# Kernel tuning notes

Hardware: AMD Instinct MI355X
Metric: run time of the kernel (lower is better)

The kernel has to match this reference:

```python
import jax, jax.numpy as jnp
import numpy as np

NUM_HEADS = 32      # query heads
NUM_KV_HEADS = 8    # GQA kv heads
HEAD_DIM = 128
BS = 16             # decode batch (one new token per sequence)
KV_LEN = 2048       # pages (page_size=1 -> tokens) per sequence
NUM_SLOTS = BS * KV_LEN
SCALE = HEAD_DIM ** -0.5


def setup_inputs() -> dict:
    key = jax.random.key(0)
    ks = jax.random.split(key, 6)
    q = jax.random.normal(ks[0], (BS, NUM_HEADS * HEAD_DIM), dtype=jnp.float32)
    k = jax.random.normal(ks[1], (BS, NUM_KV_HEADS * HEAD_DIM), dtype=jnp.float32)
    v = jax.random.normal(ks[2], (BS, NUM_KV_HEADS * HEAD_DIM), dtype=jnp.float32)
    k_cache = jax.random.normal(ks[3], (NUM_SLOTS, NUM_KV_HEADS * HEAD_DIM), dtype=jnp.float32)
    v_cache = jax.random.normal(ks[4], (NUM_SLOTS, NUM_KV_HEADS * HEAD_DIM), dtype=jnp.float32)
    # paged layout: each sequence owns KV_LEN non-contiguous slots (page_size=1)
    perm = jax.random.permutation(ks[5], NUM_SLOTS).astype(jnp.int32)
    page_indices = perm.reshape(BS, KV_LEN)            # [BS, KV_LEN] slot ids
    slot_mapping = page_indices[:, -1]                 # new token written to last page
    return {"q": q, "k": k, "v": v, "k_cache": k_cache, "v_cache": v_cache,
            "slot_mapping": slot_mapping, "page_indices": page_indices}


def reference(q, k, v, k_cache, v_cache, slot_mapping, page_indices):
    # store_kvcache: scatter new K/V rows into flat [num_slots, Hkv*d] caches
    k_cache = k_cache.at[slot_mapping].set(k)
    v_cache = v_cache.at[slot_mapping].set(v)
    # paged gather (page_size=1): [BS, KV_LEN, Hkv, d]
    keys = k_cache[page_indices].reshape(BS, KV_LEN, NUM_KV_HEADS, HEAD_DIM)
    vals = v_cache[page_indices].reshape(BS, KV_LEN, NUM_KV_HEADS, HEAD_DIM)
    # GQA: query head h uses kv head h // group
    group = NUM_HEADS // NUM_KV_HEADS
    qh = q.reshape(BS, NUM_KV_HEADS, group, HEAD_DIM)
    scores = jnp.einsum('bhgd,blhd->bhgl', qh, keys) * SCALE   # [BS,Hkv,g,L]
    p = jax.nn.softmax(scores, axis=-1)
    o = jnp.einsum('bhgl,blhd->bhgd', p, vals)                 # [BS,Hkv,g,d]
    return o.reshape(BS, NUM_HEADS * HEAD_DIM)
```

## Files before the change

### kernel.cpp

```cpp
#include <hip/hip_runtime.h>
#include <math.h>

constexpr int NUM_HEADS    = 32;
constexpr int NUM_KV_HEADS = 8;
constexpr int HEAD_DIM     = 128;
constexpr int BS           = 16;
constexpr int KV_LEN       = 2048;
constexpr int GROUP        = NUM_HEADS / NUM_KV_HEADS;
constexpr int NCHUNK       = 8;
constexpr int CHUNK        = KV_LEN / NCHUNK;

__global__ __launch_bounds__(256, 4) void attn_partial_kernel(
    const float* __restrict__ q,
    const float* __restrict__ knew,
    const float* __restrict__ vnew,
    const float* __restrict__ k_cache,
    const float* __restrict__ v_cache,
    const int*   __restrict__ page_indices,
    float* __restrict__ ws_o,
    float* __restrict__ ws_m,
    float* __restrict__ ws_s)
{
    const int bid   = blockIdx.x;
    const int chunk = bid % NCHUNK;
    const int h     = (bid / NCHUNK) % NUM_KV_HEADS;
    const int b     = bid / (NCHUNK * NUM_KV_HEADS);

    const int tid  = threadIdx.x;
    const int wid  = tid >> 6;
    const int lane = tid & 63;
    const int g    = lane >> 4;
    const int sub  = lane & 15;

    const float qscale = 0.08838834764831845f * 1.4426950408889634f;

    float qv[GROUP][8];
#pragma unroll
    for (int hg = 0; hg < GROUP; ++hg) {
        const float* qp = q + ((size_t)b * NUM_HEADS + h * GROUP + hg) * HEAD_DIM;
        const float4 a = *(const float4*)(qp + sub * 4);
        const float4 c = *(const float4*)(qp + 64 + sub * 4);
        qv[hg][0] = a.x * qscale; qv[hg][1] = a.y * qscale;
        qv[hg][2] = a.z * qscale; qv[hg][3] = a.w * qscale;
        qv[hg][4] = c.x * qscale; qv[hg][5] = c.y * qscale;
        qv[hg][6] = c.z * qscale; qv[hg][7] = c.w * qscale;
    }

    float m[GROUP], ssum[GROUP], o[GROUP][8];
#pragma unroll
    for (int hg = 0; hg < GROUP; ++hg) {
        m[hg] = -INFINITY; ssum[hg] = 0.f;
#pragma unroll
        for (int j = 0; j < 8; ++j) o[hg][j] = 0.f;
    }

    const int lbase = chunk * CHUNK;
    const float* knew_row = knew + ((size_t)b * NUM_KV_HEADS + h) * HEAD_DIM;
    const float* vnew_row = vnew + ((size_t)b * NUM_KV_HEADS + h) * HEAD_DIM;

    for (int it = 0; it < CHUNK / 16; ++it) {
        const int l   = lbase + it * 16 + wid * 4 + g;
        const int idx = page_indices[b * KV_LEN + l];

        const float* kr;
        const float* vr;
        if (l == KV_LEN - 1) {
            kr = knew_row; vr = vnew_row;
        } else {
            kr = k_cache + ((size_t)idx * NUM_KV_HEADS + h) * HEAD_DIM;
            vr = v_cache + ((size_t)idx * NUM_KV_HEADS + h) * HEAD_DIM;
        }
        const float4 k0 = *(const float4*)(kr + sub * 4);
        const float4 k1 = *(const float4*)(kr + 64 + sub * 4);
        const float4 v0 = *(const float4*)(vr + sub * 4);
        const float4 v1 = *(const float4*)(vr + 64 + sub * 4);

        float sc[GROUP];
#pragma unroll
        for (int hg = 0; hg < GROUP; ++hg) {
            sc[hg] = qv[hg][0] * k0.x + qv[hg][1] * k0.y + qv[hg][2] * k0.z + qv[hg][3] * k0.w
                   + qv[hg][4] * k1.x + qv[hg][5] * k1.y + qv[hg][6] * k1.z + qv[hg][7] * k1.w;
        }
#pragma unroll
        for (int off = 1; off < 16; off <<= 1) {
#pragma unroll
            for (int hg = 0; hg < GROUP; ++hg)
                sc[hg] += __shfl_xor(sc[hg], off, 64);
        }
#pragma unroll
        for (int hg = 0; hg < GROUP; ++hg) {
            const float mn = fmaxf(m[hg], sc[hg]);
            const float cf = exp2f(m[hg] - mn);
            const float pr = exp2f(sc[hg] - mn);
            ssum[hg] = ssum[hg] * cf + pr;
            m[hg] = mn;
            o[hg][0] = o[hg][0] * cf + pr * v0.x;
            o[hg][1] = o[hg][1] * cf + pr * v0.y;
            o[hg][2] = o[hg][2] * cf + pr * v0.z;
            o[hg][3] = o[hg][3] * cf + pr * v0.w;
            o[hg][4] = o[hg][4] * cf + pr * v1.x;
            o[hg][5] = o[hg][5] * cf + pr * v1.y;
            o[hg][6] = o[hg][6] * cf + pr * v1.z;
            o[hg][7] = o[hg][7] * cf + pr * v1.w;
        }
    }

#pragma unroll
    for (int off = 16; off <= 32; off <<= 1) {
#pragma unroll
        for (int hg = 0; hg < GROUP; ++hg) {
            const float mo = __shfl_xor(m[hg], off, 64);
            const float so = __shfl_xor(ssum[hg], off, 64);
            float oo[8];
#pragma unroll
            for (int j = 0; j < 8; ++j) oo[j] = __shfl_xor(o[hg][j], off, 64);
            const float mn = fmaxf(m[hg], mo);
            const float c1 = exp2f(m[hg] - mn);
            const float c2 = exp2f(mo - mn);
            ssum[hg] = ssum[hg] * c1 + so * c2;
#pragma unroll
            for (int j = 0; j < 8; ++j) o[hg][j] = o[hg][j] * c1 + oo[j] * c2;
            m[hg] = mn;
        }
    }

    __shared__ float red_o[4][GROUP][HEAD_DIM];
    __shared__ float red_m[4][GROUP];
    __shared__ float red_s[4][GROUP];
    if (lane < 16) {
#pragma unroll
        for (int hg = 0; hg < GROUP; ++hg) {
            *(float4*)&red_o[wid][hg][sub * 4]      = make_float4(o[hg][0], o[hg][1], o[hg][2], o[hg][3]);
            *(float4*)&red_o[wid][hg][64 + sub * 4] = make_float4(o[hg][4], o[hg][5], o[hg][6], o[hg][7]);
        }
        if (sub == 0) {
#pragma unroll
            for (int hg = 0; hg < GROUP; ++hg) { red_m[wid][hg] = m[hg]; red_s[wid][hg] = ssum[hg]; }
        }
    }
    __syncthreads();

    if (wid == 0) {
        const int hg = g;
        const float mn = fmaxf(fmaxf(red_m[0][hg], red_m[1][hg]),
                               fmaxf(red_m[2][hg], red_m[3][hg]));
        float stot = 0.f;
        float acc[8] = {0.f,0.f,0.f,0.f,0.f,0.f,0.f,0.f};
#pragma unroll
        for (int w = 0; w < 4; ++w) {
            const float c = exp2f(red_m[w][hg] - mn);
            stot += red_s[w][hg] * c;
#pragma unroll
            for (int j = 0; j < 4; ++j) acc[j]     += red_o[w][hg][sub * 4 + j] * c;
#pragma unroll
            for (int j = 0; j < 4; ++j) acc[4 + j] += red_o[w][hg][64 + sub * 4 + j] * c;
        }
        const size_t pbase = (((size_t)chunk * BS + b) * NUM_KV_HEADS + h) * GROUP + hg;
        float* op = ws_o + pbase * HEAD_DIM;
        *(float4*)(op + sub * 4)      = make_float4(acc[0], acc[1], acc[2], acc[3]);
        *(float4*)(op + 64 + sub * 4) = make_float4(acc[4], acc[5], acc[6], acc[7]);
        if (sub == 0) { ws_m[pbase] = mn; ws_s[pbase] = stot; }
    }
}

__global__ __launch_bounds__(128) void attn_combine_kernel(
    const float* __restrict__ ws_o,
    const float* __restrict__ ws_m,
    const float* __restrict__ ws_s,
    float* __restrict__ out)
{
    const int bid = blockIdx.x;
    const int hg  = bid % GROUP;
    const int h   = (bid / GROUP) % NUM_KV_HEADS;
    const int b   = bid / (GROUP * NUM_KV_HEADS);
    const int d   = threadIdx.x;

    float mv[NCHUNK];
    float mx = -INFINITY;
#pragma unroll
    for (int c = 0; c < NCHUNK; ++c) {
        mv[c] = ws_m[(((size_t)c * BS + b) * NUM_KV_HEADS + h) * GROUP + hg];
        mx = fmaxf(mx, mv[c]);
    }
    float stot = 0.f, acc = 0.f;
#pragma unroll
    for (int c = 0; c < NCHUNK; ++c) {
        const size_t pbase = (((size_t)c * BS + b) * NUM_KV_HEADS + h) * GROUP + hg;
        const float cf = exp2f(mv[c] - mx);
        stot += ws_s[pbase] * cf;
        acc  += ws_o[pbase * HEAD_DIM + d] * cf;
    }
    out[((size_t)b * NUM_HEADS + h * GROUP + hg) * HEAD_DIM + d] = acc / stot;
}

extern "C" void kernel_launch(void* const* d_in, const int* in_sizes, int n_in,
                              void* d_out, int out_size, void* d_ws, size_t ws_size,
                              hipStream_t stream)
{
    const float* q       = (const float*)d_in[0];
    const float* k       = (const float*)d_in[1];
    const float* v       = (const float*)d_in[2];
    const float* k_cache = (const float*)d_in[3];
    const float* v_cache = (const float*)d_in[4];
    const int* page_indices = (const int*)d_in[6];
    float* out = (float*)d_out;

    float* ws_o = (float*)d_ws;
    float* ws_m = ws_o + (size_t)NCHUNK * BS * NUM_KV_HEADS * GROUP * HEAD_DIM;
    float* ws_s = ws_m + (size_t)NCHUNK * BS * NUM_KV_HEADS * GROUP;

    attn_partial_kernel<<<BS * NUM_KV_HEADS * NCHUNK, 256, 0, stream>>>(
        q, k, v, k_cache, v_cache, page_indices, ws_o, ws_m, ws_s);
    attn_combine_kernel<<<BS * NUM_KV_HEADS * GROUP, 128, 0, stream>>>(
        ws_o, ws_m, ws_s, out);
}
```

Measured before the change: 50.71 us.

## Double the KV split, preload page indices, and software-prefetch next K/V rows

Doubles the number of KV chunks to 16, which halves the per-block loop length and doubles the grid to 2048 blocks for more memory parallelism. All page indices a thread needs are loaded into registers up front, and the loop is fully unrolled with the next iteration's K/V float4 loads issued before the current iteration's compute. The goal is to hide gather latency on the random paged accesses. In exchange it raises register pressure, which could limit occupancy under launch_bounds(256,4), and doubles the partial workspace that the combine kernel reads.

```diff
diff --git a/kernel.cpp b/kernel.cpp
--- a/kernel.cpp
+++ b/kernel.cpp
@@ -7,8 +7,9 @@
 constexpr int BS           = 16;
 constexpr int KV_LEN       = 2048;
 constexpr int GROUP        = NUM_HEADS / NUM_KV_HEADS;
-constexpr int NCHUNK       = 8;
+constexpr int NCHUNK       = 16;
 constexpr int CHUNK        = KV_LEN / NCHUNK;
+constexpr int NIT          = CHUNK / 16;
 
 __global__ __launch_bounds__(256, 4) void attn_partial_kernel(
     const float* __restrict__ q,
@@ -31,6 +32,14 @@
     const int lane = tid & 63;
     const int g    = lane >> 4;
     const int sub  = lane & 15;
+    const int lg   = wid * 4 + g;
+
+    const int lbase = chunk * CHUNK;
+
+    int idxr[NIT];
+#pragma unroll
+    for (int it = 0; it < NIT; ++it)
+        idxr[it] = page_indices[b * KV_LEN + lbase + it * 16 + lg];
 
     const float qscale = 0.08838834764831845f * 1.4426950408889634f;
 
@@ -46,34 +55,47 @@
         qv[hg][6] = c.z * qscale; qv[hg][7] = c.w * qscale;
     }
 
-    float m[GROUP], ssum[GROUP], o[GROUP][8];
-#pragma unroll
-    for (int hg = 0; hg < GROUP; ++hg) {
-        m[hg] = -INFINITY; ssum[hg] = 0.f;
-#pragma unroll
-        for (int j = 0; j < 8; ++j) o[hg][j] = 0.f;
-    }
-
-    const int lbase = chunk * CHUNK;
     const float* knew_row = knew + ((size_t)b * NUM_KV_HEADS + h) * HEAD_DIM;
     const float* vnew_row = vnew + ((size_t)b * NUM_KV_HEADS + h) * HEAD_DIM;
 
-    for (int it = 0; it < CHUNK / 16; ++it) {
-        const int l   = lbase + it * 16 + wid * 4 + g;
-        const int idx = page_indices[b * KV_LEN + l];
-
-        const float* kr;
-        const float* vr;
+    auto make_ptrs = [&](int it, const float*& kr, const float*& vr) {
+        const int l   = lbase + it * 16 + lg;
+        const int idx = idxr[it];
         if (l == KV_LEN - 1) {
             kr = knew_row; vr = vnew_row;
         } else {
             kr = k_cache + ((size_t)idx * NUM_KV_HEADS + h) * HEAD_DIM;
             vr = v_cache + ((size_t)idx * NUM_KV_HEADS + h) * HEAD_DIM;
         }
-        const float4 k0 = *(const float4*)(kr + sub * 4);
-        const float4 k1 = *(const float4*)(kr + 64 + sub * 4);
-        const float4 v0 = *(const float4*)(vr + sub * 4);
-        const float4 v1 = *(const float4*)(vr + 64 + sub * 4);
+    };
+
+    float m[GROUP], ssum[GROUP], o[GROUP][8];
+#pragma unroll
+    for (int hg = 0; hg < GROUP; ++hg) {
+        m[hg] = -INFINITY; ssum[hg] = 0.f;
+#pragma unroll
+        for (int j = 0; j < 8; ++j) o[hg][j] = 0.f;
+    }
+
+    float4 k0, k1, v0, v1;
+    {
+        const float *kr, *vr; make_ptrs(0, kr, vr);
+        k0 = *(const float4*)(kr + sub * 4);
+        k1 = *(const float4*)(kr + 64 + sub * 4);
+        v0 = *(const float4*)(vr + sub * 4);
+        v1 = *(const float4*)(vr + 64 + sub * 4);
+    }
+
+#pragma unroll
+    for (int it = 0; it < NIT; ++it) {
+        float4 nk0, nk1, nv0, nv1;
+        if (it + 1 < NIT) {
+            const float *kr, *vr; make_ptrs(it + 1, kr, vr);
+            nk0 = *(const float4*)(kr + sub * 4);
+            nk1 = *(const float4*)(kr + 64 + sub * 4);
+            nv0 = *(const float4*)(vr + sub * 4);
+            nv1 = *(const float4*)(vr + 64 + sub * 4);
+        }
 
         float sc[GROUP];
 #pragma unroll
@@ -103,6 +125,8 @@
             o[hg][6] = o[hg][6] * cf + pr * v1.z;
             o[hg][7] = o[hg][7] * cf + pr * v1.w;
         }
+
+        if (it + 1 < NIT) { k0 = nk0; k1 = nk1; v0 = nv0; v1 = nv1; }
     }
 
 #pragma unroll
```

Measured after the change: 122.0 us. +140.6%, slower.

## Stage full KV rows into LDS via async global_load_lds with double buffering

Applied to the files above, without the earlier changes.

Each block now covers one sequence and chunk across all 8 KV heads, with one wave per head. Whole K/V cache rows (all heads) are copied into LDS using global_load_lds DMA, double-buffered, with page indices prefetched one step ahead. The aim is to read each page row contiguously, overlap memory traffic with compute, and cut redundant index loads. In exchange there is a block-wide barrier every 4 positions and an extra cross-wave reduction in the combine step, since NCHUNK grows to 32 and per-wave partials are written straight out.

```diff
diff --git a/kernel.cpp b/kernel.cpp
--- a/kernel.cpp
+++ b/kernel.cpp
@@ -7,10 +7,20 @@
 constexpr int BS           = 16;
 constexpr int KV_LEN       = 2048;
 constexpr int GROUP        = NUM_HEADS / NUM_KV_HEADS;
-constexpr int NCHUNK       = 8;
+constexpr int NCHUNK       = 32;
 constexpr int CHUNK        = KV_LEN / NCHUNK;
-
-__global__ __launch_bounds__(256, 4) void attn_partial_kernel(
+constexpr int TPOS         = 4;
+constexpr int NT           = CHUNK / TPOS;
+constexpr int ROWF         = NUM_KV_HEADS * HEAD_DIM;
+constexpr int POSSTRIDE    = 2 * ROWF + 8;
+
+__device__ __forceinline__ void dma16(const float* g, float* l) {
+    __builtin_amdgcn_global_load_lds(
+        (const __attribute__((address_space(1))) void*)g,
+        (__attribute__((address_space(3))) void*)l, 16, 0, 0);
+}
+
+__global__ __launch_bounds__(512, 2) void attn_partial_kernel(
     const float* __restrict__ q,
     const float* __restrict__ knew,
     const float* __restrict__ vnew,
@@ -23,14 +33,20 @@
 {
     const int bid   = blockIdx.x;
     const int chunk = bid % NCHUNK;
-    const int h     = (bid / NCHUNK) % NUM_KV_HEADS;
-    const int b     = bid / (NCHUNK * NUM_KV_HEADS);
+    const int b     = bid / NCHUNK;
 
     const int tid  = threadIdx.x;
     const int wid  = tid >> 6;
     const int lane = tid & 63;
     const int g    = lane >> 4;
     const int sub  = lane & 15;
+    const int h    = wid;
+    const int arr  = wid >> 2;
+    const int quar = wid & 3;
+
+    const int lbase = chunk * CHUNK;
+
+    __shared__ float smem[2][TPOS][POSSTRIDE];
 
     const float qscale = 0.08838834764831845f * 1.4426950408889634f;
 
@@ -54,26 +70,48 @@
         for (int j = 0; j < 8; ++j) o[hg][j] = 0.f;
     }
 
-    const int lbase = chunk * CHUNK;
-    const float* knew_row = knew + ((size_t)b * NUM_KV_HEADS + h) * HEAD_DIM;
-    const float* vnew_row = vnew + ((size_t)b * NUM_KV_HEADS + h) * HEAD_DIM;
-
-    for (int it = 0; it < CHUNK / 16; ++it) {
-        const int l   = lbase + it * 16 + wid * 4 + g;
-        const int idx = page_indices[b * KV_LEN + l];
-
-        const float* kr;
-        const float* vr;
-        if (l == KV_LEN - 1) {
-            kr = knew_row; vr = vnew_row;
-        } else {
-            kr = k_cache + ((size_t)idx * NUM_KV_HEADS + h) * HEAD_DIM;
-            vr = v_cache + ((size_t)idx * NUM_KV_HEADS + h) * HEAD_DIM;
-        }
-        const float4 k0 = *(const float4*)(kr + sub * 4);
-        const float4 k1 = *(const float4*)(kr + 64 + sub * 4);
-        const float4 v0 = *(const float4*)(vr + sub * 4);
-        const float4 v1 = *(const float4*)(vr + 64 + sub * 4);
+    const float* kcnew = knew + (size_t)b * ROWF;
+    const float* vcnew = vnew + (size_t)b * ROWF;
+
+    auto stage = [&](int buf, int t, const int idx[TPOS]) {
+#pragma unroll
+        for (int j = 0; j < TPOS; ++j) {
+            const int l = lbase + t * TPOS + j;
+            const float* src;
+            if (l == KV_LEN - 1)
+                src = arr ? vcnew : kcnew;
+            else
+                src = (arr ? v_cache : k_cache) + (size_t)idx[j] * ROWF;
+            dma16(src + quar * 256 + lane * 4,
+                  &smem[buf][j][arr * ROWF + quar * 256]);
+        }
+    };
+
+    int nidx[TPOS];
+#pragma unroll
+    for (int j = 0; j < TPOS; ++j) nidx[j] = page_indices[b * KV_LEN + lbase + j];
+    stage(0, 0, nidx);
+#pragma unroll
+    for (int j = 0; j < TPOS; ++j) nidx[j] = page_indices[b * KV_LEN + lbase + TPOS + j];
+
+#pragma unroll 1
+    for (int t = 0; t < NT; ++t) {
+        __syncthreads();
+
+        if (t + 1 < NT) {
+            stage((t + 1) & 1, t + 1, nidx);
+            if (t + 2 < NT) {
+#pragma unroll
+                for (int j = 0; j < TPOS; ++j)
+                    nidx[j] = page_indices[b * KV_LEN + lbase + (t + 2) * TPOS + j];
+            }
+        }
+
+        const float* bp = &smem[t & 1][g][0];
+        const float4 k0 = *(const float4*)(bp + h * HEAD_DIM + sub * 4);
+        const float4 k1 = *(const float4*)(bp + h * HEAD_DIM + 64 + sub * 4);
+        const float4 v0 = *(const float4*)(bp + ROWF + h * HEAD_DIM + sub * 4);
+        const float4 v1 = *(const float4*)(bp + ROWF + h * HEAD_DIM + 64 + sub * 4);
 
         float sc[GROUP];
 #pragma unroll
@@ -124,42 +162,18 @@
         }
     }
 
-    __shared__ float red_o[4][GROUP][HEAD_DIM];
-    __shared__ float red_m[4][GROUP];
-    __shared__ float red_s[4][GROUP];
     if (lane < 16) {
-#pragma unroll
-        for (int hg = 0; hg < GROUP; ++hg) {
-            *(float4*)&red_o[wid][hg][sub * 4]      = make_float4(o[hg][0], o[hg][1], o[hg][2], o[hg][3]);
-            *(float4*)&red_o[wid][hg][64 + sub * 4] = make_float4(o[hg][4], o[hg][5], o[hg][6], o[hg][7]);
+        const size_t pb0 = (((size_t)chunk * BS + b) * NUM_KV_HEADS + h) * GROUP;
+#pragma unroll
+        for (int hg = 0; hg < GROUP; ++hg) {
+            float* op = ws_o + (pb0 + hg) * HEAD_DIM;
+            *(float4*)(op + sub * 4)      = make_float4(o[hg][0], o[hg][1], o[hg][2], o[hg][3]);
+            *(float4*)(op + 64 + sub * 4) = make_float4(o[hg][4], o[hg][5], o[hg][6], o[hg][7]);
         }
         if (sub == 0) {
 #pragma unroll
-            for (int hg = 0; hg < GROUP; ++hg) { red_m[wid][hg] = m[hg]; red_s[wid][hg] = ssum[hg]; }
-        }
-    }
-    __syncthreads();
-
-    if (wid == 0) {
-        const int hg = g;
-        const float mn = fmaxf(fmaxf(red_m[0][hg], red_m[1][hg]),
-                               fmaxf(red_m[2][hg], red_m[3][hg]));
-        float stot = 0.f;
-        float acc[8] = {0.f,0.f,0.f,0.f,0.f,0.f,0.f,0.f};
-#pragma unroll
-        for (int w = 0; w < 4; ++w) {
-            const float c = exp2f(red_m[w][hg] - mn);
-            stot += red_s[w][hg] * c;
-#pragma unroll
-            for (int j = 0; j < 4; ++j) acc[j]     += red_o[w][hg][sub * 4 + j] * c;
-#pragma unroll
-            for (int j = 0; j < 4; ++j) acc[4 + j] += red_o[w][hg][64 + sub * 4 + j] * c;
-        }
-        const size_t pbase = (((size_t)chunk * BS + b) * NUM_KV_HEADS + h) * GROUP + hg;
-        float* op = ws_o + pbase * HEAD_DIM;
-        *(float4*)(op + sub * 4)      = make_float4(acc[0], acc[1], acc[2], acc[3]);
-        *(float4*)(op + 64 + sub * 4) = make_float4(acc[4], acc[5], acc[6], acc[7]);
-        if (sub == 0) { ws_m[pbase] = mn; ws_s[pbase] = stot; }
+            for (int hg = 0; hg < GROUP; ++hg) { ws_m[pb0 + hg] = m[hg]; ws_s[pb0 + hg] = ssum[hg]; }
+        }
     }
 }
 
@@ -175,18 +189,17 @@
     const int b   = bid / (GROUP * NUM_KV_HEADS);
     const int d   = threadIdx.x;
 
-    float mv[NCHUNK];
     float mx = -INFINITY;
-#pragma unroll
+#pragma unroll 8
     for (int c = 0; c < NCHUNK; ++c) {
-        mv[c] = ws_m[(((size_t)c * BS + b) * NUM_KV_HEADS + h) * GROUP + hg];
-        mx = fmaxf(mx, mv[c]);
+        const float mv = ws_m[(((size_t)c * BS + b) * NUM_KV_HEADS + h) * GROUP + hg];
+        mx = fmaxf(mx, mv);
     }
     float stot = 0.f, acc = 0.f;
-#pragma unroll
+#pragma unroll 8
     for (int c = 0; c < NCHUNK; ++c) {
         const size_t pbase = (((size_t)c * BS + b) * NUM_KV_HEADS + h) * GROUP + hg;
-        const float cf = exp2f(mv[c] - mx);
+        const float cf = exp2f(ws_m[pbase] - mx);
         stot += ws_s[pbase] * cf;
         acc  += ws_o[pbase * HEAD_DIM + d] * cf;
     }
@@ -209,7 +222,7 @@
     float* ws_m = ws_o + (size_t)NCHUNK * BS * NUM_KV_HEADS * GROUP * HEAD_DIM;
     float* ws_s = ws_m + (size_t)NCHUNK * BS * NUM_KV_HEADS * GROUP;
 
-    attn_partial_kernel<<<BS * NUM_KV_HEADS * NCHUNK, 256, 0, stream>>>(
+    attn_partial_kernel<<<BS * NCHUNK, 512, 0, stream>>>(
         q, k, v, k_cache, v_cache, page_indices, ws_o, ws_m, ws_s);
     attn_combine_kernel<<<BS * NUM_KV_HEADS * GROUP, 128, 0, stream>>>(
         ws_o, ws_m, ws_s, out);
```

Result: slower. 59.85 us (+18.0%).
